# Kernel tuning notes

Hardware: AMD Instinct MI355X
Metric: run time of the kernel (lower is better)

## Reference

```python
import jax, jax.numpy as jnp
import numpy as np
import math

B, S, H, NH = 4, 1024, 1024, 16
HD = H // NH  # 64
MAX_REL = 127


def relative_position_encoding(depth, max_length, max_relative_position):
    vocab_size = max_relative_position * 2 + 1
    range_vec = np.arange(max_length)
    distance = range_vec[None, :] - range_vec[:, None]  # matches range_mat - range_mat.T
    final_mat = np.clip(distance, -max_relative_position, max_relative_position) + max_relative_position
    position = np.arange(vocab_size, dtype=np.float32)[:, None]
    div_term = np.exp(np.arange(0, depth, 2, dtype=np.float32) * (-math.log(10000.0) / depth))
    table = np.zeros((vocab_size, depth), dtype=np.float32)
    table[:, 0::2] = np.sin(position * div_term)
    table[:, 1::2] = np.cos(position * div_term)
    return jnp.asarray(table[final_mat])  # [max_length, max_length, depth]


def setup_inputs() -> dict:
    key = jax.random.key(0)
    ks = jax.random.split(key, 4)
    sc = 0.02
    return {
        "hidden_states": jax.random.normal(ks[0], (B, S, H), dtype=jnp.float32),
        "Wq": jax.random.normal(ks[1], (H, H), dtype=jnp.float32) * sc,
        "bq": jnp.zeros((H,), dtype=jnp.float32),
        "Wk": jax.random.normal(ks[2], (H, H), dtype=jnp.float32) * sc,
        "bk": jnp.zeros((H,), dtype=jnp.float32),
        "Wv": jax.random.normal(ks[3], (H, H), dtype=jnp.float32) * sc,
        "bv": jnp.zeros((H,), dtype=jnp.float32),
        "rel_pos": relative_position_encoding(HD, S, MAX_REL),  # [S, S, HD] sinusoidal buffer
    }


def reference(hidden_states, Wq, bq, Wk, bk, Wv, bv, rel_pos):
    b, s, h = hidden_states.shape

    def heads(x):  # [b,s,h] -> [b,nh,s,hd]
        return x.reshape(b, s, NH, HD).transpose(0, 2, 1, 3)

    q = heads(hidden_states @ Wq.T + bq)
    k = heads(hidden_states @ Wk.T + bk)
    v = heads(hidden_states @ Wv.T + bv)

    scores = jnp.einsum("bhqd,bhkd->bhqk", q, k)
    # query-relative-key positional term
    scores = scores + jnp.einsum("bhqd,qkd->bhqk", q, rel_pos)
    scores = scores / math.sqrt(HD)

    probs = jax.nn.softmax(scores, axis=-1)  # dropout p=0 (eval)

    ctx = jnp.einsum("bhqk,bhkd->bhqd", probs, v)
    # prob-relative-value positional term
    ctx = ctx + jnp.einsum("bhqk,qkd->bhqd", probs, rel_pos)

    return ctx.transpose(0, 2, 1, 3).reshape(b, s, h)
```

## Files before the change

kernel.cpp:

```cpp
#include <hip/hip_runtime.h>
#include <stdint.h>


typedef __bf16 bf16x8 __attribute__((ext_vector_type(8)));
typedef float f32x4 __attribute__((ext_vector_type(4)));
typedef uint16_t u16x8 __attribute__((ext_vector_type(8)));
typedef uint16_t u16x4 __attribute__((ext_vector_type(4)));

__device__ __forceinline__ uint16_t f2bf(float f) {
    uint32_t u = __builtin_bit_cast(uint32_t, f);
    return (uint16_t)((u + 0x7FFFu + ((u >> 16) & 1u)) >> 16);
}
__device__ __forceinline__ float bf2f(uint16_t h) {
    uint32_t u = ((uint32_t)h) << 16;
    return __builtin_bit_cast(float, u);
}
__device__ __forceinline__ f32x4 mfma16(bf16x8 a, bf16x8 b, f32x4 c) {
    return __builtin_amdgcn_mfma_f32_16x16x32_bf16(a, b, c, 0, 0, 0);
}
__device__ __forceinline__ bf16x8 ldg8(const uint16_t* p) {
    return __builtin_bit_cast(bf16x8, *(const u16x8*)p);
}
__device__ __forceinline__ bf16x8 lds8(const uint16_t* base, int byteoff) {
    return __builtin_bit_cast(bf16x8, *(const u16x8*)((const char*)base + byteoff));
}

__global__ void k_cast_all(const float* __restrict__ hs, const float* __restrict__ wq,
                           const float* __restrict__ wk, const float* __restrict__ wv,
                           uint16_t* __restrict__ hs_bf, uint16_t* __restrict__ w_bf) {
    int b = blockIdx.x;
    const float* src;
    uint16_t* dst;
    int i;
    if (b < 2048)      { src = hs; dst = hs_bf;           i = b * 256 + threadIdx.x; }
    else if (b < 2560) { src = wq; dst = w_bf;            i = (b - 2048) * 256 + threadIdx.x; }
    else if (b < 3072) { src = wk; dst = w_bf + 1048576;  i = (b - 2560) * 256 + threadIdx.x; }
    else               { src = wv; dst = w_bf + 2097152;  i = (b - 3072) * 256 + threadIdx.x; }
    float4 a = ((const float4*)src)[2 * i];
    float4 c = ((const float4*)src)[2 * i + 1];
    u16x8 o;
    o[0] = f2bf(a.x); o[1] = f2bf(a.y); o[2] = f2bf(a.z); o[3] = f2bf(a.w);
    o[4] = f2bf(c.x); o[5] = f2bf(c.y); o[6] = f2bf(c.z); o[7] = f2bf(c.w);
    ((u16x8*)dst)[i] = o;
}

__global__ void k_table(const float* __restrict__ rel, uint16_t* __restrict__ tab,
                        uint16_t* __restrict__ tabT) {
    int idx = blockIdx.x * 256 + threadIdx.x;
    int j = idx >> 6, d = idx & 63;
    float v = 0.0f;
    if (j < 255) v = rel[((size_t)512 * 1024 + (512 + j - 127)) * 64 + d];
    uint16_t h = f2bf(v);
    tab[j * 64 + d] = h;
    tabT[d * 256 + j] = h;
}

__launch_bounds__(256)
__global__ void k_gemm_qkv3(const uint16_t* __restrict__ A, const uint16_t* __restrict__ Wt,
                            const float* __restrict__ bq, const float* __restrict__ bk,
                            const float* __restrict__ bvp, uint16_t* __restrict__ qout,
                            uint16_t* __restrict__ kout, uint16_t* __restrict__ vt) {
    __shared__ uint16_t As[128 * 64];
    __shared__ uint16_t Bs[128 * 64];
    int bid = blockIdx.x;
    int swz = (bid & 7) * 96 + (bid >> 3);
    int m0 = (swz & 31) * 128, n0 = (swz >> 5) * 128;
    int tid = threadIdx.x;
    int w = tid >> 6, l = tid & 63, lg = l >> 4, ln = l & 15;
    int wm = w >> 1, wn = w & 1;
    int lrow = tid >> 3, lcol = (tid & 7) * 8;
    f32x4 acc[4][4] = {};
    for (int kt = 0; kt < 16; ++kt) {
        int k0 = kt * 64;
        __syncthreads();
#pragma unroll
        for (int c = 0; c < 4; ++c) {
            int row = c * 32 + lrow;
            __builtin_amdgcn_global_load_lds(
                (const __attribute__((address_space(1))) void*)(A + (size_t)(m0 + row) * 1024 + k0 + lcol),
                (__attribute__((address_space(3))) void*)&As[row * 64 + lcol], 16, 0, 0);
            __builtin_amdgcn_global_load_lds(
                (const __attribute__((address_space(1))) void*)(Wt + (size_t)(n0 + row) * 1024 + k0 + lcol),
                (__attribute__((address_space(3))) void*)&Bs[row * 64 + lcol], 16, 0, 0);
        }
        __syncthreads();
#pragma unroll
        for (int ks = 0; ks < 2; ++ks) {
            bf16x8 af[4], bfr[4];
#pragma unroll
            for (int mi = 0; mi < 4; ++mi)
                af[mi] = ldg8(&As[(wm * 64 + mi * 16 + ln) * 64 + ks * 32 + lg * 8]);
#pragma unroll
            for (int ni = 0; ni < 4; ++ni)
                bfr[ni] = ldg8(&Bs[(wn * 64 + ni * 16 + ln) * 64 + ks * 32 + lg * 8]);
#pragma unroll
            for (int mi = 0; mi < 4; ++mi)
#pragma unroll
                for (int ni = 0; ni < 4; ++ni)
                    acc[mi][ni] = mfma16(af[mi], bfr[ni], acc[mi][ni]);
        }
    }
    int b = m0 >> 10, srow = (m0 & 1023) + wm * 64;
#pragma unroll
    for (int ni = 0; ni < 4; ++ni) {
        int n = n0 + wn * 64 + ni * 16 + ln;
        int which = n >> 10, nr = n & 1023;
        const float* bp = which == 0 ? bq : (which == 1 ? bk : bvp);
        float bb = bp[nr];
        int h = nr >> 6, d = nr & 63;
        if (which < 2) {
            uint16_t* base = which == 0 ? qout : kout;
#pragma unroll
            for (int mi = 0; mi < 4; ++mi)
#pragma unroll
                for (int r = 0; r < 4; ++r) {
                    int s = srow + mi * 16 + lg * 4 + r;
                    base[(((size_t)(b * 16 + h)) * 1024 + s) * 64 + d] = f2bf(acc[mi][ni][r] + bb);
                }
        } else {
#pragma unroll
            for (int mi = 0; mi < 4; ++mi) {
                int s0 = srow + mi * 16 + lg * 4;
                u16x4 pv;
#pragma unroll
                for (int r = 0; r < 4; ++r) pv[r] = f2bf(acc[mi][ni][r] + bb);
                *(u16x4*)&vt[(((size_t)(b * 16 + h)) * 64 + d) * 1024 + s0] = pv;
            }
        }
    }
}

__launch_bounds__(256)
__global__ void k_r_gemm(const uint16_t* __restrict__ q, const uint16_t* __restrict__ tab,
                         uint16_t* __restrict__ R) {
    __shared__ uint16_t Qs[64 * 72];
    int m0 = blockIdx.x * 64;
    int tid = threadIdx.x;
    int w = tid >> 6, l = tid & 63, lg = l >> 4, ln = l & 15;
#pragma unroll
    for (int c = 0; c < 2; ++c) {
        int idx = c * 256 + tid; int row = idx >> 3, seg = idx & 7;
        *(u16x8*)&Qs[row * 72 + seg * 8] =
            *(const u16x8*)(q + (size_t)(m0 + row) * 64 + seg * 8);
    }
    __syncthreads();
    bf16x8 aq[4][2];
#pragma unroll
    for (int mi = 0; mi < 4; ++mi)
#pragma unroll
        for (int ks = 0; ks < 2; ++ks)
            aq[mi][ks] = ldg8(&Qs[(mi * 16 + ln) * 72 + ks * 32 + lg * 8]);
    f32x4 acc[4][4] = {};
#pragma unroll
    for (int ni = 0; ni < 4; ++ni) {
        int j = w * 64 + ni * 16 + ln;
#pragma unroll
        for (int ks = 0; ks < 2; ++ks) {
            bf16x8 bt = ldg8(tab + j * 64 + ks * 32 + lg * 8);
#pragma unroll
            for (int mi = 0; mi < 4; ++mi)
                acc[mi][ni] = mfma16(aq[mi][ks], bt, acc[mi][ni]);
        }
    }
#pragma unroll
    for (int ni = 0; ni < 4; ++ni)
#pragma unroll
        for (int mi = 0; mi < 4; ++mi)
#pragma unroll
            for (int r = 0; r < 4; ++r)
                R[(size_t)(m0 + mi * 16 + lg * 4 + r) * 256 + w * 64 + ni * 16 + ln] =
                    f2bf(acc[mi][ni][r]);
}

__device__ __forceinline__ void softmax_grp(
    const f32x4 (&acc)[4], int kt, int qbase, int ln, const uint16_t* __restrict__ Rrow,
    float rel_lo, float rel_hi, uint16_t* prow, int lg,
    float& mref, float& lloc, float& slo, float& shi,
    uint32_t (&pk)[4][2], f32x4 (&oacc)[4]) {
    int cls = (kt * 64 - (qbase + 15) >= 127) ? 2
            : ((kt * 64 + 63 - qbase <= -127) ? 0 : 1);
    int qg = qbase + ln;
    float sv[16];
    if (cls == 2) {
#pragma unroll
        for (int m = 0; m < 4; ++m)
#pragma unroll
            for (int r = 0; r < 4; ++r) sv[m * 4 + r] = fmaf(acc[m][r], 0.125f, rel_hi);
    } else if (cls == 0) {
#pragma unroll
        for (int m = 0; m < 4; ++m)
#pragma unroll
            for (int r = 0; r < 4; ++r) sv[m * 4 + r] = fmaf(acc[m][r], 0.125f, rel_lo);
    } else {
#pragma unroll
        for (int m = 0; m < 4; ++m) {
            int base = kt * 64 + (m >> 1) * 32 + lg * 8 + (m & 1) * 4 - qg;
#pragma unroll
            for (int r = 0; r < 4; ++r) {
                int dj = base + r;
                int djc = dj < -127 ? -127 : (dj > 127 ? 127 : dj);
                float rel = bf2f(Rrow[djc + 127]);
                sv[m * 4 + r] = (acc[m][r] + rel) * 0.125f;
            }
        }
    }
    float t0 = fmaxf(fmaxf(sv[0], sv[1]), fmaxf(sv[2], sv[3]));
    float t1 = fmaxf(fmaxf(sv[4], sv[5]), fmaxf(sv[6], sv[7]));
    float t2 = fmaxf(fmaxf(sv[8], sv[9]), fmaxf(sv[10], sv[11]));
    float t3 = fmaxf(fmaxf(sv[12], sv[13]), fmaxf(sv[14], sv[15]));
    float tm = fmaxf(fmaxf(t0, t1), fmaxf(t2, t3));
    bool needL = tm > mref + 8.0f;
    if (__any(needL)) {
        float tmm = fmaxf(tm, __shfl_xor(tm, 16));
        tmm = fmaxf(tmm, __shfl_xor(tmm, 32));
        bool need = tmm > mref + 8.0f;
        float f = need ? __expf(mref - tmm) : 1.0f;
#pragma unroll
        for (int r = 0; r < 4; ++r) {
            float fr = __shfl(f, lg * 4 + r);
#pragma unroll
            for (int nt = 0; nt < 4; ++nt) oacc[nt][r] *= fr;
        }
        if (need) {
            lloc *= f; slo *= f; shi *= f;
            uint16_t* pr = prow + lg * 64;
#pragma unroll
            for (int c = 0; c < 8; ++c) {
                u16x8 pv8 = *(u16x8*)&pr[c * 8];
#pragma unroll
                for (int e = 0; e < 8; ++e) pv8[e] = f2bf(bf2f(pv8[e]) * f);
                *(u16x8*)&pr[c * 8] = pv8;
            }
            mref = tmm;
        }
    }
    float pm[4];
    if (cls == 1) {
#pragma unroll
        for (int m = 0; m < 4; ++m) {
            int base = kt * 64 + (m >> 1) * 32 + lg * 8 + (m & 1) * 4 - qg;
            uint32_t w0 = 0, w1 = 0;
            float ps = 0.f;
#pragma unroll
            for (int r = 0; r < 4; ++r) {
                float P = __expf(sv[m * 4 + r] - mref);
                ps += P;
                uint32_t h = f2bf(P);
                int dj = base + r;
                if (dj <= -127) slo += P;
                else if (dj >= 127) shi += P;
                else prow[dj + 127] = (uint16_t)h;
                if (r < 2) w0 |= h << (16 * r); else w1 |= h << (16 * (r - 2));
            }
            pm[m] = ps;
            pk[m][0] = w0; pk[m][1] = w1;
        }
    } else {
#pragma unroll
        for (int m = 0; m < 4; ++m) {
            uint32_t w0 = 0, w1 = 0;
            float ps = 0.f;
#pragma unroll
            for (int r = 0; r < 4; ++r) {
                float P = __expf(sv[m * 4 + r] - mref);
                ps += P;
                uint32_t h = f2bf(P);
                if (r < 2) w0 |= h << (16 * r); else w1 |= h << (16 * (r - 2));
            }
            pm[m] = ps;
            pk[m][0] = w0; pk[m][1] = w1;
        }
        float ts = (pm[0] + pm[1]) + (pm[2] + pm[3]);
        if (cls == 2) shi += ts; else slo += ts;
    }
    lloc += (pm[0] + pm[1]) + (pm[2] + pm[3]);
}

__launch_bounds__(256, 2)
__global__ void k_attn_fused(const uint16_t* __restrict__ qb, const uint16_t* __restrict__ kb,
                             const uint16_t* __restrict__ vtb, const uint16_t* __restrict__ Rb,
                             const uint16_t* __restrict__ tabT, float* __restrict__ out) {
    __shared__ uint16_t Pagg[128 * 256];
    __shared__ uint16_t Kb[64 * 64];
    __shared__ uint16_t Vb[64 * 64];
    int bid = blockIdx.x;
    bid = (bid & 7) * 64 + (bid >> 3);
    int bh = bid >> 3, q0 = (bid & 7) * 128;
    int tid = threadIdx.x;
    int w = tid >> 6, l = tid & 63, lg = l >> 4, ln = l & 15;
    int qbaseA = q0 + w * 16, qbaseB = qbaseA + 64;
    int qA = qbaseA + ln, qB = qA + 64;
    bf16x8 qfA[2], qfB[2];
    {
        const uint16_t* qr = qb + ((size_t)bh * 1024 + qA) * 64;
        qfA[0] = ldg8(qr + lg * 8); qfA[1] = ldg8(qr + 32 + lg * 8);
        qr += 64 * 64;
        qfB[0] = ldg8(qr + lg * 8); qfB[1] = ldg8(qr + 32 + lg * 8);
    }
    const uint16_t* RrowA = Rb + ((size_t)bh * 1024 + qA) * 256;
    const uint16_t* RrowB = RrowA + 64 * 256;
    uint16_t* prowA = &Pagg[(w * 16 + ln) * 256];
    uint16_t* prowB = &Pagg[(64 + w * 16 + ln) * 256];
    {
        u16x8* pa = (u16x8*)&Pagg[(w * 16) * 256];
        u16x8* pb2 = (u16x8*)&Pagg[(64 + w * 16) * 256];
#pragma unroll
        for (int i = 0; i < 8; ++i) { pa[i * 64 + l] = (u16x8)0; pb2[i * 64 + l] = (u16x8)0; }
    }
    float relA_lo = bf2f(RrowA[0]) * 0.125f, relA_hi = bf2f(RrowA[254]) * 0.125f;
    float relB_lo = bf2f(RrowB[0]) * 0.125f, relB_hi = bf2f(RrowB[254]) * 0.125f;
    const int r0 = tid >> 3, c16 = tid & 7;
    const int r1 = 32 + r0;
    const int slotK0 = (r0 & 3) | ((r0 >> 1) & 4), slotK1 = (r1 & 3) | ((r1 >> 1) & 4);
    const int waK0 = (r0 * 128 + c16 * 16) ^ (slotK0 << 4);
    const int waK1 = (r1 * 128 + c16 * 16) ^ (slotK1 << 4);
    const int waV0 = (r0 * 128 + c16 * 16) ^ ((r0 & 7) << 4);
    const int waV1 = (r1 * 128 + c16 * 16) ^ ((r1 & 7) << 4);
    const uint16_t* kt_base = kb + ((size_t)bh * 1024) * 64;
    const uint16_t* vt_base = vtb + (size_t)bh * 64 * 1024;
    u16x8 kc0 = *(const u16x8*)(kt_base + (size_t)r0 * 64 + c16 * 8);
    u16x8 kc1 = *(const u16x8*)(kt_base + (size_t)r1 * 64 + c16 * 8);
    u16x8 vc0 = *(const u16x8*)(vt_base + (size_t)r0 * 1024 + c16 * 8);
    u16x8 vc1 = *(const u16x8*)(vt_base + (size_t)r1 * 1024 + c16 * 8);
    float mrefA = -1e30f, llocA = 0.f, sloA = 0.f, shiA = 0.f;
    float mrefB = -1e30f, llocB = 0.f, sloB = 0.f, shiB = 0.f;
    f32x4 oaccA[4] = {}, oaccB[4] = {};
    for (int kt = 0; kt < 16; ++kt) {
        __syncthreads();
        *(u16x8*)((char*)Kb + waK0) = kc0;
        *(u16x8*)((char*)Kb + waK1) = kc1;
        *(u16x8*)((char*)Vb + waV0) = vc0;
        *(u16x8*)((char*)Vb + waV1) = vc1;
        __syncthreads();
        if (kt < 15) {
            const uint16_t* kn = kt_base + (size_t)(kt + 1) * 64 * 64;
            const uint16_t* vn = vt_base + (kt + 1) * 64;
            kc0 = *(const u16x8*)(kn + (size_t)r0 * 64 + c16 * 8);
            kc1 = *(const u16x8*)(kn + (size_t)r1 * 64 + c16 * 8);
            vc0 = *(const u16x8*)(vn + (size_t)r0 * 1024 + c16 * 8);
            vc1 = *(const u16x8*)(vn + (size_t)r1 * 1024 + c16 * 8);
        }
        f32x4 accA[4] = {}, accB[4] = {};
#pragma unroll
        for (int m = 0; m < 4; ++m) {
            int rowp = ((m >> 1) << 5) + ((ln >> 2) << 3) + ((m & 1) << 2) + (ln & 3);
            bf16x8 a0 = lds8(Kb, (rowp * 128 + lg * 16) ^ ((ln & 7) << 4));
            bf16x8 a1 = lds8(Kb, (rowp * 128 + 64 + lg * 16) ^ ((ln & 7) << 4));
            accA[m] = mfma16(a0, qfA[0], accA[m]);
            accA[m] = mfma16(a1, qfA[1], accA[m]);
            accB[m] = mfma16(a0, qfB[0], accB[m]);
            accB[m] = mfma16(a1, qfB[1], accB[m]);
        }
        uint32_t pkA[4][2], pkB[4][2];
        softmax_grp(accA, kt, qbaseA, ln, RrowA, relA_lo, relA_hi, prowA, lg,
                    mrefA, llocA, sloA, shiA, pkA, oaccA);
        softmax_grp(accB, kt, qbaseB, ln, RrowB, relB_lo, relB_hi, prowB, lg,
                    mrefB, llocB, sloB, shiB, pkB, oaccB);
#pragma unroll
        for (int ks = 0; ks < 2; ++ks) {
            uint32_t fa[4] = {pkA[2 * ks][0], pkA[2 * ks][1], pkA[2 * ks + 1][0], pkA[2 * ks + 1][1]};
            uint32_t fb[4] = {pkB[2 * ks][0], pkB[2 * ks][1], pkB[2 * ks + 1][0], pkB[2 * ks + 1][1]};
            bf16x8 apA = __builtin_bit_cast(bf16x8, fa);
            bf16x8 apB = __builtin_bit_cast(bf16x8, fb);
#pragma unroll
            for (int nt = 0; nt < 4; ++nt) {
                int row = nt * 16 + ln;
                bf16x8 bv = lds8(Vb, (row * 128 + (ks * 4 + lg) * 16) ^ ((ln & 7) << 4));
                oaccA[nt] = mfma16(apA, bv, oaccA[nt]);
                oaccB[nt] = mfma16(apB, bv, oaccB[nt]);
            }
        }
    }
    llocA += __shfl_xor(llocA, 16); llocA += __shfl_xor(llocA, 32);
    sloA  += __shfl_xor(sloA, 16);  sloA  += __shfl_xor(sloA, 32);
    shiA  += __shfl_xor(shiA, 16);  shiA  += __shfl_xor(shiA, 32);
    llocB += __shfl_xor(llocB, 16); llocB += __shfl_xor(llocB, 32);
    sloB  += __shfl_xor(sloB, 16);  sloB  += __shfl_xor(sloB, 32);
    shiB  += __shfl_xor(shiB, 16);  shiB  += __shfl_xor(shiB, 32);
    if (lg == 0) {
        prowA[0] = f2bf(sloA); prowA[254] = f2bf(shiA);
        prowB[0] = f2bf(sloB); prowB[254] = f2bf(shiB);
    }
#pragma unroll
    for (int ks8 = 0; ks8 < 8; ++ks8) {
        bf16x8 apA = ldg8(&Pagg[(w * 16 + ln) * 256 + ks8 * 32 + lg * 8]);
        bf16x8 apB = ldg8(&Pagg[(64 + w * 16 + ln) * 256 + ks8 * 32 + lg * 8]);
#pragma unroll
        for (int nt = 0; nt < 4; ++nt) {
            bf16x8 bt = ldg8(tabT + (size_t)(nt * 16 + ln) * 256 + ks8 * 32 + lg * 8);
            oaccA[nt] = mfma16(apA, bt, oaccA[nt]);
            oaccB[nt] = mfma16(apB, bt, oaccB[nt]);
        }
    }
    float rinvA[4], rinvB[4];
#pragma unroll
    for (int r = 0; r < 4; ++r) {
        rinvA[r] = 1.0f / __shfl(llocA, lg * 4 + r);
        rinvB[r] = 1.0f / __shfl(llocB, lg * 4 + r);
    }
    int b = bh >> 4, h = bh & 15;
#pragma unroll
    for (int nt = 0; nt < 4; ++nt) {
#pragma unroll
        for (int r = 0; r < 4; ++r) {
            int qoA = q0 + w * 16 + lg * 4 + r;
            out[((size_t)b * 1024 + qoA) * 1024 + h * 64 + nt * 16 + ln] = oaccA[nt][r] * rinvA[r];
            out[((size_t)b * 1024 + qoA + 64) * 1024 + h * 64 + nt * 16 + ln] = oaccB[nt][r] * rinvB[r];
        }
    }
}

extern "C" void kernel_launch(void* const* d_in, const int* in_sizes, int n_in,
                              void* d_out, int out_size, void* d_ws, size_t ws_size,
                              hipStream_t stream) {
    const float* hs  = (const float*)d_in[0];
    const float* Wq  = (const float*)d_in[1];
    const float* bq  = (const float*)d_in[2];
    const float* Wk  = (const float*)d_in[3];
    const float* bk  = (const float*)d_in[4];
    const float* Wv  = (const float*)d_in[5];
    const float* bv  = (const float*)d_in[6];
    const float* rel = (const float*)d_in[7];
    float* out = (float*)d_out;
    char* ws = (char*)d_ws;

    uint16_t* hs_bf = (uint16_t*)(ws);
    uint16_t* W_bf  = (uint16_t*)(ws + 8388608);
    uint16_t* q_bf  = (uint16_t*)(ws + 14680064);
    uint16_t* k_bf  = (uint16_t*)(ws + 23068672);
    uint16_t* vt_bf = (uint16_t*)(ws + 31457280);
    uint16_t* R_bf  = (uint16_t*)(ws + 48234496);
    uint16_t* tab   = (uint16_t*)(ws + 81788928);
    uint16_t* tabT  = (uint16_t*)(ws + 81821696);

    k_cast_all<<<3584, 256, 0, stream>>>(hs, Wq, Wk, Wv, hs_bf, W_bf);
    k_table<<<64, 256, 0, stream>>>(rel, tab, tabT);

    k_gemm_qkv3<<<768, 256, 0, stream>>>(hs_bf, W_bf, bq, bk, bv, q_bf, k_bf, vt_bf);
    k_r_gemm<<<1024, 256, 0, stream>>>(q_bf, tab, R_bf);

    k_attn_fused<<<512, 256, 0, stream>>>(q_bf, k_bf, vt_bf, R_bf, tabT, out);
}
```

Measured before the change: 149.3 us.

## Stage QKV GEMM epilogue through LDS and double-buffer K/V in attention with 8 waves

The QKV GEMM epilogue now writes bias-added bf16 results into a swizzled shared-memory tile and then emits 16-byte coalesced stores for Q/K and the transposed V, replacing scattered 2-byte and 8-byte stores. The attention kernel moves from 4 waves each handling two 16-row query groups to 8 waves each handling one group, which halves per-thread register state. It also double-buffers the K/V tiles in LDS so there is one barrier per iteration instead of two. The trade-offs are extra LDS traffic and barriers in the GEMM epilogue, and more LDS and larger blocks in attention, which could reduce occupancy.

```diff
diff --git a/kernel.cpp b/kernel.cpp
--- a/kernel.cpp
+++ b/kernel.cpp
@@ -21,7 +21,7 @@
 __device__ __forceinline__ bf16x8 ldg8(const uint16_t* p) {
     return __builtin_bit_cast(bf16x8, *(const u16x8*)p);
 }
-__device__ __forceinline__ bf16x8 lds8(const uint16_t* base, int byteoff) {
+__device__ __forceinline__ bf16x8 lds8(const void* base, int byteoff) {
     return __builtin_bit_cast(bf16x8, *(const u16x8*)((const char*)base + byteoff));
 }
 
@@ -60,8 +60,9 @@
                             const float* __restrict__ bq, const float* __restrict__ bk,
                             const float* __restrict__ bvp, uint16_t* __restrict__ qout,
                             uint16_t* __restrict__ kout, uint16_t* __restrict__ vt) {
-    __shared__ uint16_t As[128 * 64];
-    __shared__ uint16_t Bs[128 * 64];
+    __shared__ uint16_t Sh[2 * 128 * 64];
+    uint16_t* As = Sh;
+    uint16_t* Bs = Sh + 8192;
     int bid = blockIdx.x;
     int swz = (bid & 7) * 96 + (bid >> 3);
     int m0 = (swz & 31) * 128, n0 = (swz >> 5) * 128;
@@ -100,32 +101,60 @@
                     acc[mi][ni] = mfma16(af[mi], bfr[ni], acc[mi][ni]);
         }
     }
-    int b = m0 >> 10, srow = (m0 & 1023) + wm * 64;
-#pragma unroll
-    for (int ni = 0; ni < 4; ++ni) {
-        int n = n0 + wn * 64 + ni * 16 + ln;
-        int which = n >> 10, nr = n & 1023;
-        const float* bp = which == 0 ? bq : (which == 1 ? bk : bvp);
-        float bb = bp[nr];
-        int h = nr >> 6, d = nr & 63;
-        if (which < 2) {
-            uint16_t* base = which == 0 ? qout : kout;
+    int b = m0 >> 10, s0r = m0 & 1023;
+    int which = n0 >> 10, nbase = n0 & 1023;
+    __syncthreads();
+    if (which < 2) {
+        uint16_t* qk = which == 0 ? qout : kout;
+        const float* bp = which == 0 ? bq : bk;
+#pragma unroll
+        for (int ni = 0; ni < 4; ++ni) {
+            int d2 = wn * 64 + ni * 16 + ln;
+            float bb = bp[nbase + d2];
 #pragma unroll
             for (int mi = 0; mi < 4; ++mi)
 #pragma unroll
                 for (int r = 0; r < 4; ++r) {
-                    int s = srow + mi * 16 + lg * 4 + r;
-                    base[(((size_t)(b * 16 + h)) * 1024 + s) * 64 + d] = f2bf(acc[mi][ni][r] + bb);
+                    int s2 = wm * 64 + mi * 16 + lg * 4 + r;
+                    *(uint16_t*)((char*)Sh + ((s2 * 256 + d2 * 2) ^ (((s2 >> 2) & 7) << 4))) =
+                        f2bf(acc[mi][ni][r] + bb);
                 }
-        } else {
+        }
+        __syncthreads();
+#pragma unroll
+        for (int hh = 0; hh < 2; ++hh) {
+            int h = (nbase >> 6) + hh;
+#pragma unroll
+            for (int i = 0; i < 4; ++i) {
+                int s2 = i * 32 + w * 8 + (l >> 3);
+                int d2 = hh * 64 + (l & 7) * 8;
+                u16x8 vv = *(u16x8*)((char*)Sh + ((s2 * 256 + d2 * 2) ^ (((s2 >> 2) & 7) << 4)));
+                *(u16x8*)&qk[(((size_t)(b * 16 + h)) * 1024 + s0r + s2) * 64 + (d2 & 63)] = vv;
+            }
+        }
+    } else {
+#pragma unroll
+        for (int ni = 0; ni < 4; ++ni) {
+            int d2 = wn * 64 + ni * 16 + ln;
+            float bb = bvp[nbase + d2];
 #pragma unroll
             for (int mi = 0; mi < 4; ++mi) {
-                int s0 = srow + mi * 16 + lg * 4;
+                int s2 = wm * 64 + mi * 16 + lg * 4;
                 u16x4 pv;
 #pragma unroll
                 for (int r = 0; r < 4; ++r) pv[r] = f2bf(acc[mi][ni][r] + bb);
-                *(u16x4*)&vt[(((size_t)(b * 16 + h)) * 64 + d) * 1024 + s0] = pv;
-            }
+                *(u16x4*)((char*)Sh + ((d2 * 256 + s2 * 2) ^ ((d2 & 7) << 4))) = pv;
+            }
+        }
+        __syncthreads();
+#pragma unroll
+        for (int i = 0; i < 8; ++i) {
+            int d2 = i * 16 + w * 4 + (l >> 4);
+            int s2 = (l & 15) * 8;
+            u16x8 vv = *(u16x8*)((char*)Sh + ((d2 * 256 + s2 * 2) ^ ((d2 & 7) << 4)));
+            int nr = nbase + d2;
+            int h = nr >> 6, d = nr & 63;
+            *(u16x8*)&vt[(((size_t)(b * 16 + h)) * 64 + d) * 1024 + s0r + s2] = vv;
         }
     }
 }
@@ -276,136 +305,114 @@
     lloc += (pm[0] + pm[1]) + (pm[2] + pm[3]);
 }
 
-__launch_bounds__(256, 2)
+__launch_bounds__(512, 2)
 __global__ void k_attn_fused(const uint16_t* __restrict__ qb, const uint16_t* __restrict__ kb,
                              const uint16_t* __restrict__ vtb, const uint16_t* __restrict__ Rb,
                              const uint16_t* __restrict__ tabT, float* __restrict__ out) {
     __shared__ uint16_t Pagg[128 * 256];
-    __shared__ uint16_t Kb[64 * 64];
-    __shared__ uint16_t Vb[64 * 64];
+    __shared__ uint16_t Kb[2 * 64 * 64];
+    __shared__ uint16_t Vb[2 * 64 * 64];
     int bid = blockIdx.x;
     bid = (bid & 7) * 64 + (bid >> 3);
     int bh = bid >> 3, q0 = (bid & 7) * 128;
     int tid = threadIdx.x;
     int w = tid >> 6, l = tid & 63, lg = l >> 4, ln = l & 15;
-    int qbaseA = q0 + w * 16, qbaseB = qbaseA + 64;
-    int qA = qbaseA + ln, qB = qA + 64;
-    bf16x8 qfA[2], qfB[2];
+    int qbase = q0 + w * 16;
+    int qg = qbase + ln;
+    bf16x8 qf[2];
     {
-        const uint16_t* qr = qb + ((size_t)bh * 1024 + qA) * 64;
-        qfA[0] = ldg8(qr + lg * 8); qfA[1] = ldg8(qr + 32 + lg * 8);
-        qr += 64 * 64;
-        qfB[0] = ldg8(qr + lg * 8); qfB[1] = ldg8(qr + 32 + lg * 8);
-    }
-    const uint16_t* RrowA = Rb + ((size_t)bh * 1024 + qA) * 256;
-    const uint16_t* RrowB = RrowA + 64 * 256;
-    uint16_t* prowA = &Pagg[(w * 16 + ln) * 256];
-    uint16_t* prowB = &Pagg[(64 + w * 16 + ln) * 256];
+        const uint16_t* qr = qb + ((size_t)bh * 1024 + qg) * 64;
+        qf[0] = ldg8(qr + lg * 8);
+        qf[1] = ldg8(qr + 32 + lg * 8);
+    }
+    const uint16_t* Rrow = Rb + ((size_t)bh * 1024 + qg) * 256;
+    uint16_t* prow = &Pagg[(w * 16 + ln) * 256];
     {
-        u16x8* pa = (u16x8*)&Pagg[(w * 16) * 256];
-        u16x8* pb2 = (u16x8*)&Pagg[(64 + w * 16) * 256];
-#pragma unroll
-        for (int i = 0; i < 8; ++i) { pa[i * 64 + l] = (u16x8)0; pb2[i * 64 + l] = (u16x8)0; }
-    }
-    float relA_lo = bf2f(RrowA[0]) * 0.125f, relA_hi = bf2f(RrowA[254]) * 0.125f;
-    float relB_lo = bf2f(RrowB[0]) * 0.125f, relB_hi = bf2f(RrowB[254]) * 0.125f;
-    const int r0 = tid >> 3, c16 = tid & 7;
-    const int r1 = 32 + r0;
-    const int slotK0 = (r0 & 3) | ((r0 >> 1) & 4), slotK1 = (r1 & 3) | ((r1 >> 1) & 4);
-    const int waK0 = (r0 * 128 + c16 * 16) ^ (slotK0 << 4);
-    const int waK1 = (r1 * 128 + c16 * 16) ^ (slotK1 << 4);
-    const int waV0 = (r0 * 128 + c16 * 16) ^ ((r0 & 7) << 4);
-    const int waV1 = (r1 * 128 + c16 * 16) ^ ((r1 & 7) << 4);
+        u16x8* pb = (u16x8*)&Pagg[(w * 16) * 256];
+#pragma unroll
+        for (int i = 0; i < 8; ++i) pb[i * 64 + l] = (u16x8)0;
+    }
+    float rel_lo = bf2f(Rrow[0]) * 0.125f, rel_hi = bf2f(Rrow[254]) * 0.125f;
+    const int rk = tid >> 3, c16 = tid & 7;
+    const int slotK = (rk & 3) | ((rk >> 1) & 4);
+    const int waK = (rk * 128 + c16 * 16) ^ (slotK << 4);
+    const int waV = (rk * 128 + c16 * 16) ^ ((rk & 7) << 4);
     const uint16_t* kt_base = kb + ((size_t)bh * 1024) * 64;
     const uint16_t* vt_base = vtb + (size_t)bh * 64 * 1024;
-    u16x8 kc0 = *(const u16x8*)(kt_base + (size_t)r0 * 64 + c16 * 8);
-    u16x8 kc1 = *(const u16x8*)(kt_base + (size_t)r1 * 64 + c16 * 8);
-    u16x8 vc0 = *(const u16x8*)(vt_base + (size_t)r0 * 1024 + c16 * 8);
-    u16x8 vc1 = *(const u16x8*)(vt_base + (size_t)r1 * 1024 + c16 * 8);
-    float mrefA = -1e30f, llocA = 0.f, sloA = 0.f, shiA = 0.f;
-    float mrefB = -1e30f, llocB = 0.f, sloB = 0.f, shiB = 0.f;
-    f32x4 oaccA[4] = {}, oaccB[4] = {};
+    {
+        u16x8 kc = *(const u16x8*)(kt_base + (size_t)rk * 64 + c16 * 8);
+        u16x8 vc = *(const u16x8*)(vt_base + (size_t)rk * 1024 + c16 * 8);
+        *(u16x8*)((char*)Kb + waK) = kc;
+        *(u16x8*)((char*)Vb + waV) = vc;
+    }
+    __syncthreads();
+    float mref = -1e30f, lloc = 0.f, slo = 0.f, shi = 0.f;
+    f32x4 oacc[4] = {};
+    int cur = 0;
     for (int kt = 0; kt < 16; ++kt) {
-        __syncthreads();
-        *(u16x8*)((char*)Kb + waK0) = kc0;
-        *(u16x8*)((char*)Kb + waK1) = kc1;
-        *(u16x8*)((char*)Vb + waV0) = vc0;
-        *(u16x8*)((char*)Vb + waV1) = vc1;
-        __syncthreads();
+        u16x8 kcN, vcN;
         if (kt < 15) {
-            const uint16_t* kn = kt_base + (size_t)(kt + 1) * 64 * 64;
-            const uint16_t* vn = vt_base + (kt + 1) * 64;
-            kc0 = *(const u16x8*)(kn + (size_t)r0 * 64 + c16 * 8);
-            kc1 = *(const u16x8*)(kn + (size_t)r1 * 64 + c16 * 8);
-            vc0 = *(const u16x8*)(vn + (size_t)r0 * 1024 + c16 * 8);
-            vc1 = *(const u16x8*)(vn + (size_t)r1 * 1024 + c16 * 8);
-        }
-        f32x4 accA[4] = {}, accB[4] = {};
+            kcN = *(const u16x8*)(kt_base + (size_t)(kt + 1) * 4096 + (size_t)rk * 64 + c16 * 8);
+            vcN = *(const u16x8*)(vt_base + (size_t)rk * 1024 + (kt + 1) * 64 + c16 * 8);
+        }
+        const char* Kcur = (const char*)Kb + cur * 8192;
+        const char* Vcur = (const char*)Vb + cur * 8192;
+        f32x4 acc[4] = {};
 #pragma unroll
         for (int m = 0; m < 4; ++m) {
             int rowp = ((m >> 1) << 5) + ((ln >> 2) << 3) + ((m & 1) << 2) + (ln & 3);
-            bf16x8 a0 = lds8(Kb, (rowp * 128 + lg * 16) ^ ((ln & 7) << 4));
-            bf16x8 a1 = lds8(Kb, (rowp * 128 + 64 + lg * 16) ^ ((ln & 7) << 4));
-            accA[m] = mfma16(a0, qfA[0], accA[m]);
-            accA[m] = mfma16(a1, qfA[1], accA[m]);
-            accB[m] = mfma16(a0, qfB[0], accB[m]);
-            accB[m] = mfma16(a1, qfB[1], accB[m]);
-        }
-        uint32_t pkA[4][2], pkB[4][2];
-        softmax_grp(accA, kt, qbaseA, ln, RrowA, relA_lo, relA_hi, prowA, lg,
-                    mrefA, llocA, sloA, shiA, pkA, oaccA);
-        softmax_grp(accB, kt, qbaseB, ln, RrowB, relB_lo, relB_hi, prowB, lg,
-                    mrefB, llocB, sloB, shiB, pkB, oaccB);
+            bf16x8 a0 = lds8(Kcur, (rowp * 128 + lg * 16) ^ ((ln & 7) << 4));
+            bf16x8 a1 = lds8(Kcur, (rowp * 128 + 64 + lg * 16) ^ ((ln & 7) << 4));
+            acc[m] = mfma16(a0, qf[0], acc[m]);
+            acc[m] = mfma16(a1, qf[1], acc[m]);
+        }
+        uint32_t pk[4][2];
+        softmax_grp(acc, kt, qbase, ln, Rrow, rel_lo, rel_hi, prow, lg,
+                    mref, lloc, slo, shi, pk, oacc);
 #pragma unroll
         for (int ks = 0; ks < 2; ++ks) {
-            uint32_t fa[4] = {pkA[2 * ks][0], pkA[2 * ks][1], pkA[2 * ks + 1][0], pkA[2 * ks + 1][1]};
-            uint32_t fb[4] = {pkB[2 * ks][0], pkB[2 * ks][1], pkB[2 * ks + 1][0], pkB[2 * ks + 1][1]};
-            bf16x8 apA = __builtin_bit_cast(bf16x8, fa);
-            bf16x8 apB = __builtin_bit_cast(bf16x8, fb);
+            uint32_t fa[4] = {pk[2 * ks][0], pk[2 * ks][1], pk[2 * ks + 1][0], pk[2 * ks + 1][1]};
+            bf16x8 ap = __builtin_bit_cast(bf16x8, fa);
 #pragma unroll
             for (int nt = 0; nt < 4; ++nt) {
                 int row = nt * 16 + ln;
-                bf16x8 bv = lds8(Vb, (row * 128 + (ks * 4 + lg) * 16) ^ ((ln & 7) << 4));
-                oaccA[nt] = mfma16(apA, bv, oaccA[nt]);
-                oaccB[nt] = mfma16(apB, bv, oaccB[nt]);
-            }
-        }
-    }
-    llocA += __shfl_xor(llocA, 16); llocA += __shfl_xor(llocA, 32);
-    sloA  += __shfl_xor(sloA, 16);  sloA  += __shfl_xor(sloA, 32);
-    shiA  += __shfl_xor(shiA, 16);  shiA  += __shfl_xor(shiA, 32);
-    llocB += __shfl_xor(llocB, 16); llocB += __shfl_xor(llocB, 32);
-    sloB  += __shfl_xor(sloB, 16);  sloB  += __shfl_xor(sloB, 32);
-    shiB  += __shfl_xor(shiB, 16);  shiB  += __shfl_xor(shiB, 32);
+                bf16x8 bv = lds8(Vcur, (row * 128 + (ks * 4 + lg) * 16) ^ ((ln & 7) << 4));
+                oacc[nt] = mfma16(ap, bv, oacc[nt]);
+            }
+        }
+        if (kt < 15) {
+            *(u16x8*)((char*)Kb + (cur ^ 1) * 8192 + waK) = kcN;
+            *(u16x8*)((char*)Vb + (cur ^ 1) * 8192 + waV) = vcN;
+            __syncthreads();
+            cur ^= 1;
+        }
+    }
+    lloc += __shfl_xor(lloc, 16); lloc += __shfl_xor(lloc, 32);
+    slo  += __shfl_xor(slo, 16);  slo  += __shfl_xor(slo, 32);
+    shi  += __shfl_xor(shi, 16);  shi  += __shfl_xor(shi, 32);
     if (lg == 0) {
-        prowA[0] = f2bf(sloA); prowA[254] = f2bf(shiA);
-        prowB[0] = f2bf(sloB); prowB[254] = f2bf(shiB);
+        prow[0]   = f2bf(slo);
+        prow[254] = f2bf(shi);
     }
 #pragma unroll
     for (int ks8 = 0; ks8 < 8; ++ks8) {
-        bf16x8 apA = ldg8(&Pagg[(w * 16 + ln) * 256 + ks8 * 32 + lg * 8]);
-        bf16x8 apB = ldg8(&Pagg[(64 + w * 16 + ln) * 256 + ks8 * 32 + lg * 8]);
+        bf16x8 ap = ldg8(&Pagg[(w * 16 + ln) * 256 + ks8 * 32 + lg * 8]);
 #pragma unroll
         for (int nt = 0; nt < 4; ++nt) {
             bf16x8 bt = ldg8(tabT + (size_t)(nt * 16 + ln) * 256 + ks8 * 32 + lg * 8);
-            oaccA[nt] = mfma16(apA, bt, oaccA[nt]);
-            oaccB[nt] = mfma16(apB, bt, oaccB[nt]);
-        }
-    }
-    float rinvA[4], rinvB[4];
-#pragma unroll
-    for (int r = 0; r < 4; ++r) {
-        rinvA[r] = 1.0f / __shfl(llocA, lg * 4 + r);
-        rinvB[r] = 1.0f / __shfl(llocB, lg * 4 + r);
-    }
+            oacc[nt] = mfma16(ap, bt, oacc[nt]);
+        }
+    }
+    float rinv[4];
+#pragma unroll
+    for (int r = 0; r < 4; ++r) rinv[r] = 1.0f / __shfl(lloc, lg * 4 + r);
     int b = bh >> 4, h = bh & 15;
 #pragma unroll
     for (int nt = 0; nt < 4; ++nt) {
 #pragma unroll
         for (int r = 0; r < 4; ++r) {
-            int qoA = q0 + w * 16 + lg * 4 + r;
-            out[((size_t)b * 1024 + qoA) * 1024 + h * 64 + nt * 16 + ln] = oaccA[nt][r] * rinvA[r];
-            out[((size_t)b * 1024 + qoA + 64) * 1024 + h * 64 + nt * 16 + ln] = oaccB[nt][r] * rinvB[r];
+            int qo = q0 + w * 16 + lg * 4 + r;
+            out[((size_t)b * 1024 + qo) * 1024 + h * 64 + nt * 16 + ln] = oacc[nt][r] * rinv[r];
         }
     }
 }
@@ -439,5 +446,5 @@
     k_gemm_qkv3<<<768, 256, 0, stream>>>(hs_bf, W_bf, bq, bk, bv, q_bf, k_bf, vt_bf);
     k_r_gemm<<<1024, 256, 0, stream>>>(q_bf, tab, R_bf);
 
-    k_attn_fused<<<512, 256, 0, stream>>>(q_bf, k_bf, vt_bf, R_bf, tabT, out);
-}
+    k_attn_fused<<<512, 512, 0, stream>>>(q_bf, k_bf, vt_bf, R_bf, tabT, out);
+}
```

Result: slower. 167.4 us (+12.1%).
